# Kernel optimization log

Hardware: AMD Instinct MI355X
Metric: run time of the kernel (lower is better)

## Reference

```python
import jax, jax.numpy as jnp
import numpy as np

WIN = 7
NUM_HEADS = 12
DIM = 384
HEAD_DIM = DIM // NUM_HEADS
SEQ = WIN * WIN


def _relative_position_index():
    ch, cw = np.meshgrid(np.arange(WIN), np.arange(WIN), indexing='ij')
    coords = np.stack([ch, cw]).reshape(2, -1)            # [2, 49]
    rel = coords[:, :, None] - coords[:, None, :]          # [2, 49, 49]
    rel = rel.transpose(1, 2, 0)
    rel[:, :, 0] += WIN - 1
    rel[:, :, 1] += WIN - 1
    rel[:, :, 0] *= 2 * WIN - 1
    return rel.sum(-1).astype(np.int32)                    # [49, 49]


def setup_inputs() -> dict:
    key = jax.random.key(0)
    ks = jax.random.split(key, 12)
    bz = 2048
    mw = 64  # windows per image
    s = 0.02
    inp = {
        'hidden_states': jax.random.normal(ks[0], (bz, SEQ, DIM), jnp.float32),
        'attention_mask': jax.random.normal(ks[1], (mw, SEQ, SEQ), jnp.float32),
        'qW': jax.random.normal(ks[2], (DIM, DIM), jnp.float32) * s,
        'qb': jnp.zeros((DIM,), jnp.float32),
        'kW': jax.random.normal(ks[3], (DIM, DIM), jnp.float32) * s,
        'kb': jnp.zeros((DIM,), jnp.float32),
        'vW': jax.random.normal(ks[4], (DIM, DIM), jnp.float32) * s,
        'vb': jnp.zeros((DIM,), jnp.float32),
        'oW': jax.random.normal(ks[5], (DIM, DIM), jnp.float32) * s,
        'ob': jnp.zeros((DIM,), jnp.float32),
        'bias_table': jax.random.normal(ks[6], ((2 * WIN - 1) ** 2, NUM_HEADS), jnp.float32) * s,
        'rel_idx': jnp.asarray(_relative_position_index()),
    }
    return inp


def reference(hidden_states, attention_mask, qW, qb, kW, kb, vW, vb, oW, ob, bias_table, rel_idx):
    bz, seq, dim = hidden_states.shape
    H, D = NUM_HEADS, HEAD_DIM

    def heads(x, W, b):
        y = jnp.einsum('bsd,de->bse', hidden_states, W) + b
        return y.reshape(bz, seq, H, D).transpose(0, 2, 1, 3)  # [b, h, s, d]

    q = heads(hidden_states, qW, qb)
    k = heads(hidden_states, kW, kb)
    v = heads(hidden_states, vW, vb)

    scores = jnp.einsum('bhsd,bhtd->bhst', q, k) / jnp.sqrt(jnp.float32(D))

    # relative position bias: gather [49*49, H] -> [H, 49, 49]
    rpb = bias_table[rel_idx.reshape(-1)].reshape(seq, seq, H).transpose(2, 0, 1)
    scores = scores + rpb[None]

    mw = attention_mask.shape[0]
    scores = scores.reshape(bz // mw, mw, H, seq, seq) + attention_mask[None, :, None]
    scores = scores.reshape(bz, H, seq, seq)

    attn = jax.nn.softmax(scores, axis=-1)
    ctx = jnp.einsum('bhst,bhtd->bhsd', attn, v)
    ctx = ctx.transpose(0, 2, 1, 3).reshape(bz, seq, dim)
    return jnp.einsum('bsd,de->bse', ctx, oW) + ob
```

## Files before the change

### kernel.cpp

```cpp
#include <hip/hip_runtime.h>


typedef unsigned short u16;
typedef unsigned int   u32;
typedef short bf16x8 __attribute__((ext_vector_type(8)));
typedef float f32x4  __attribute__((ext_vector_type(4)));
typedef u16   u16x8  __attribute__((ext_vector_type(8)));
typedef u16   u16x4  __attribute__((ext_vector_type(4)));

#define NWIN   2048
#define SEQ    49
#define DIM    384
#define NH     12
#define HD     32
#define MTOT   (NWIN*SEQ)
#define WELEM  (DIM*DIM)

__device__ __forceinline__ u16 f2b(float f) {
    union { float f; unsigned u; } c; c.f = f;
    unsigned u = c.u;
    u += 0x7FFFu + ((u >> 16) & 1u);
    return (u16)(u >> 16);
}

__global__ __launch_bounds__(256) void prep_x(const float* __restrict__ X, u16* __restrict__ Xb) {
    int i = blockIdx.x * 256 + threadIdx.x;
    float4 v = ((const float4*)X)[i];
    u16x4 o; o[0]=f2b(v.x); o[1]=f2b(v.y); o[2]=f2b(v.z); o[3]=f2b(v.w);
    ((u16x4*)Xb)[i] = o;
}

__global__ __launch_bounds__(256) void prep_w(const float* __restrict__ qW, const float* __restrict__ kW,
                                              const float* __restrict__ vW, const float* __restrict__ oW,
                                              u16* __restrict__ Wt) {
    int t = blockIdx.x * 256 + threadIdx.x;
    int m = t / WELEM; int rem = t - m * WELEM;
    int k = rem / DIM; int n = rem - k * DIM;
    const float* src = (m==0) ? qW : (m==1) ? kW : (m==2) ? vW : oW;
    Wt[m*WELEM + n*DIM + k] = f2b(src[rem]);
}

__global__ __launch_bounds__(256) void prep_rpb(const float* __restrict__ bt, const int* __restrict__ ridx,
                                                float* __restrict__ rpb) {
    int t = blockIdx.x * 256 + threadIdx.x;
    if (t >= NH * SEQ * SEQ) return;
    int h = t / (SEQ*SEQ); int st = t - h * (SEQ*SEQ);
    rpb[t] = bt[ridx[st] * NH + h];
}

__device__ __forceinline__ void gload_lds16(const void* g, void* l) {
    __builtin_amdgcn_global_load_lds((const __attribute__((address_space(1))) void*)g,
                                     (__attribute__((address_space(3))) void*)l, 16, 0, 0);
}

__device__ __forceinline__ void stage_tile_async(const u16* __restrict__ g0, u16* lds, int wv, int lane) {
    const int r8   = lane >> 3;
    const int scol = ((lane & 7) * 8) ^ (r8 << 3);
    const u16* src = g0 + (wv * 8 + r8) * DIM + scol;
    u16*       dst = lds + wv * 512 + lane * 8;
    #pragma unroll
    for (int i = 0; i < 4; i++)
        gload_lds16(src + i * 32 * DIM, dst + i * 2048);
}

__device__ __forceinline__ void gemm_tile(const u16* __restrict__ Abase, const u16* __restrict__ Bbase,
                                          f32x4 (&acc)[4][4]) {
    __shared__ __align__(16) u16 As[128 * 64];
    __shared__ __align__(16) u16 Bs[128 * 64];
    const int tid = threadIdx.x, wave = tid >> 6, lane = tid & 63;
    const int wm = wave >> 1, wn = wave & 1;
    const int swzl = (lane & 7) << 3;
    for (int kt = 0; kt < 6; kt++) {
        __syncthreads();
        stage_tile_async(Abase + kt * 64, As, wave, lane);
        stage_tile_async(Bbase + kt * 64, Bs, wave, lane);
        __syncthreads();
        #pragma unroll
        for (int kk = 0; kk < 2; kk++) {
            const int co = (kk * 32 + (lane >> 4) * 8) ^ swzl;
            bf16x8 a[4], b[4];
            #pragma unroll
            for (int mi = 0; mi < 4; mi++)
                a[mi] = *(const bf16x8*)&As[(wm * 64 + mi * 16 + (lane & 15)) * 64 + co];
            #pragma unroll
            for (int ni = 0; ni < 4; ni++)
                b[ni] = *(const bf16x8*)&Bs[(wn * 64 + ni * 16 + (lane & 15)) * 64 + co];
            #pragma unroll
            for (int mi = 0; mi < 4; mi++)
                #pragma unroll
                for (int ni = 0; ni < 4; ni++)
                    acc[mi][ni] = __builtin_amdgcn_mfma_f32_16x16x32_bf16(a[mi], b[ni], acc[mi][ni], 0, 0, 0);
        }
    }
}

__global__ __launch_bounds__(256) void qkv_gemm(const u16* __restrict__ Xb, const u16* __restrict__ Wt,
                                                const float* __restrict__ qb, const float* __restrict__ kb,
                                                const float* __restrict__ vb,
                                                u16* __restrict__ Qo, u16* __restrict__ Ko, u16* __restrict__ Vo) {
    const int bid = blockIdx.x;
    const int swz = (bid & 7) * 882 + (bid >> 3);
    const int mTile = swz / 9, p = swz - mTile * 9;
    const int mBase = mTile * 128;
    const int proj = p / 3, nBase = (p - proj * 3) * 128;
    f32x4 acc[4][4];
    #pragma unroll
    for (int mi = 0; mi < 4; mi++)
        #pragma unroll
        for (int ni = 0; ni < 4; ni++) { f32x4 z = {0.f,0.f,0.f,0.f}; acc[mi][ni] = z; }

    gemm_tile(Xb + mBase * DIM, Wt + proj * WELEM + nBase * DIM, acc);

    const float* bias = (proj==0) ? qb : (proj==1) ? kb : vb;
    u16* Out          = (proj==0) ? Qo : (proj==1) ? Ko : Vo;
    const float scale = (proj==0) ? 0.17677669529663687f : 1.0f;
    const int tid = threadIdx.x, wave = tid >> 6, lane = tid & 63;
    const int wm = wave >> 1, wn = wave & 1;

    float bias4[4]; int hh[4], dd[4];
    #pragma unroll
    for (int ni = 0; ni < 4; ni++) {
        int nin = nBase + wn * 64 + ni * 16 + (lane & 15);
        bias4[ni] = bias[nin]; hh[ni] = nin >> 5; dd[ni] = nin & 31;
    }
    #pragma unroll
    for (int mi = 0; mi < 4; mi++) {
        #pragma unroll
        for (int j = 0; j < 4; j++) {
            int gm = mBase + wm * 64 + mi * 16 + ((lane >> 4) << 2) + j;
            int bw = gm / SEQ, s = gm - bw * SEQ;
            int rowbase = (bw * (NH*SEQ) + s) * HD;
            #pragma unroll
            for (int ni = 0; ni < 4; ni++) {
                float val = (acc[mi][ni][j] + bias4[ni]) * scale;
                Out[rowbase + hh[ni] * (SEQ*HD) + dd[ni]] = f2b(val);
            }
        }
    }
}

__global__ __launch_bounds__(256) void attn_mfma(const u16* __restrict__ Qb, const u16* __restrict__ Kb,
                                                 const u16* __restrict__ Vb, const float* __restrict__ rpb,
                                                 const float* __restrict__ mask, u16* __restrict__ Ctx) {
    const int wm = blockIdx.x;
    const int h  = blockIdx.y;
    const int jg = blockIdx.z;
    const int tid = threadIdx.x, wv = tid >> 6, lane = tid & 63;
    const int r16 = lane & 15, g = lane >> 4;

    __shared__ float comb[64][68];
    {
        const float* rp = rpb + h * (SEQ*SEQ);
        const float* mp = mask + wm * (SEQ*SEQ);
        for (int idx = tid; idx < 64*64; idx += 256) {
            int s = idx >> 6, t = idx & 63;
            float v = -1e30f;
            if (s < SEQ && t < SEQ) v = rp[s*SEQ + t] + mp[s*SEQ + t];
            comb[s][t] = v;
        }
    }
    __syncthreads();

    const int j = jg * 4 + wv;
    const int w = j * 64 + wm;
    const u16* Qp = Qb + (w*NH + h) * (SEQ*HD);
    const u16* Kp = Kb + (w*NH + h) * (SEQ*HD);
    const u16* Vp = Vb + (w*NH + h) * (SEQ*HD);

    bf16x8 kf[4], qf[4];
    #pragma unroll
    for (int ti = 0; ti < 4; ti++) kf[ti] = *(const bf16x8*)&Kp[(ti*16 + r16)*HD + g*8];
    #pragma unroll
    for (int si = 0; si < 4; si++) qf[si] = *(const bf16x8*)&Qp[(si*16 + r16)*HD + g*8];

    f32x4 st[4][4];
    #pragma unroll
    for (int ti = 0; ti < 4; ti++)
        #pragma unroll
        for (int si = 0; si < 4; si++) {
            f32x4 z = {0.f,0.f,0.f,0.f};
            st[ti][si] = __builtin_amdgcn_mfma_f32_16x16x32_bf16(kf[ti], qf[si], z, 0, 0, 0);
        }

    #pragma unroll
    for (int ti = 0; ti < 4; ti++)
        #pragma unroll
        for (int si = 0; si < 4; si++) {
            const float4 c = *(const float4*)&comb[si*16 + r16][ti*16 + g*4];
            st[ti][si][0] += c.x; st[ti][si][1] += c.y; st[ti][si][2] += c.z; st[ti][si][3] += c.w;
        }

    #pragma unroll
    for (int si = 0; si < 4; si++) {
        float m = st[0][si][0];
        #pragma unroll
        for (int ti = 0; ti < 4; ti++)
            #pragma unroll
            for (int r = 0; r < 4; r++) m = fmaxf(m, st[ti][si][r]);
        m = fmaxf(m, __shfl_xor(m, 16));
        m = fmaxf(m, __shfl_xor(m, 32));
        float sum = 0.f;
        #pragma unroll
        for (int ti = 0; ti < 4; ti++)
            #pragma unroll
            for (int r = 0; r < 4; r++) {
                float p = __expf(st[ti][si][r] - m);
                st[ti][si][r] = p; sum += p;
            }
        sum += __shfl_xor(sum, 16);
        sum += __shfl_xor(sum, 32);
        float rs = 1.0f / sum;
        #pragma unroll
        for (int ti = 0; ti < 4; ti++)
            #pragma unroll
            for (int r = 0; r < 4; r++) st[ti][si][r] *= rs;
    }

    u32 pk[4][4][2];
    #pragma unroll
    for (int ti = 0; ti < 4; ti++)
        #pragma unroll
        for (int si = 0; si < 4; si++)
            #pragma unroll
            for (int q = 0; q < 2; q++) {
                u32 r;
                asm("v_cvt_pk_bf16_f32 %0, %1, %2" : "=v"(r) : "v"(st[ti][si][2*q]), "v"(st[ti][si][2*q+1]));
                pk[ti][si][q] = r;
            }

    bf16x8 pa[2][4];
    const int base_src = r16 + ((g & 1) << 5);
    #pragma unroll
    for (int kc = 0; kc < 2; kc++)
        #pragma unroll
        for (int si = 0; si < 4; si++) {
            union { u32 u[4]; bf16x8 v; } cv;
            #pragma unroll
            for (int jj = 0; jj < 4; jj++) {
                int srcl = base_src + ((jj >> 1) << 4);
                u32 x0 = (u32)__shfl((int)pk[kc*2 + 0][si][jj & 1], srcl);
                u32 x1 = (u32)__shfl((int)pk[kc*2 + 1][si][jj & 1], srcl);
                cv.u[jj] = (lane >= 32) ? x1 : x0;
            }
            pa[kc][si] = cv.v;
        }

    bf16x8 vf[2][2];
    #pragma unroll
    for (int kc = 0; kc < 2; kc++)
        #pragma unroll
        for (int nt = 0; nt < 2; nt++) {
            bf16x8 v;
            #pragma unroll
            for (int i = 0; i < 8; i++)
                v[i] = (short)Vp[(kc*32 + g*8 + i)*HD + nt*16 + r16];
            vf[kc][nt] = v;
        }

    f32x4 ct[4][2];
    #pragma unroll
    for (int si = 0; si < 4; si++)
        #pragma unroll
        for (int nt = 0; nt < 2; nt++) {
            f32x4 z = {0.f,0.f,0.f,0.f};
            z = __builtin_amdgcn_mfma_f32_16x16x32_bf16(pa[0][si], vf[0][nt], z, 0, 0, 0);
            ct[si][nt] = __builtin_amdgcn_mfma_f32_16x16x32_bf16(pa[1][si], vf[1][nt], z, 0, 0, 0);
        }

    #pragma unroll
    for (int si = 0; si < 4; si++)
        #pragma unroll
        for (int r = 0; r < 4; r++) {
            int s = si*16 + g*4 + r;
            if (s < SEQ) {
                #pragma unroll
                for (int nt = 0; nt < 2; nt++)
                    Ctx[(w*SEQ + s)*DIM + h*HD + nt*16 + r16] = f2b(ct[si][nt][r]);
            }
        }
}

__global__ __launch_bounds__(256) void oproj_gemm(const u16* __restrict__ Cb, const u16* __restrict__ Wo,
                                                  const float* __restrict__ ob, float* __restrict__ out) {
    const int bid = blockIdx.x;
    const int swz = (bid & 7) * 294 + (bid >> 3);
    const int mTile = swz / 3, nTile = swz - mTile * 3;
    const int mBase = mTile * 128, nBase = nTile * 128;
    f32x4 acc[4][4];
    #pragma unroll
    for (int mi = 0; mi < 4; mi++)
        #pragma unroll
        for (int ni = 0; ni < 4; ni++) { f32x4 z = {0.f,0.f,0.f,0.f}; acc[mi][ni] = z; }

    gemm_tile(Cb + mBase * DIM, Wo + nBase * DIM, acc);

    const int tid = threadIdx.x, wave = tid >> 6, lane = tid & 63;
    const int wm = wave >> 1, wn = wave & 1;
    float ob4[4]; int gn4[4];
    #pragma unroll
    for (int ni = 0; ni < 4; ni++) {
        gn4[ni] = nBase + wn * 64 + ni * 16 + (lane & 15);
        ob4[ni] = ob[gn4[ni]];
    }
    #pragma unroll
    for (int mi = 0; mi < 4; mi++) {
        #pragma unroll
        for (int j = 0; j < 4; j++) {
            int gm = mBase + wm * 64 + mi * 16 + ((lane >> 4) << 2) + j;
            #pragma unroll
            for (int ni = 0; ni < 4; ni++)
                out[gm * DIM + gn4[ni]] = acc[mi][ni][j] + ob4[ni];
        }
    }
}

extern "C" void kernel_launch(void* const* d_in, const int* in_sizes, int n_in,
                              void* d_out, int out_size, void* d_ws, size_t ws_size,
                              hipStream_t stream) {
    const float* hs   = (const float*)d_in[0];
    const float* mask = (const float*)d_in[1];
    const float* qW   = (const float*)d_in[2];
    const float* qb   = (const float*)d_in[3];
    const float* kW   = (const float*)d_in[4];
    const float* kb   = (const float*)d_in[5];
    const float* vW   = (const float*)d_in[6];
    const float* vb   = (const float*)d_in[7];
    const float* oW   = (const float*)d_in[8];
    const float* ob   = (const float*)d_in[9];
    const float* bt   = (const float*)d_in[10];
    const int*   ridx = (const int*)d_in[11];
    float* out = (float*)d_out;

    char* ws = (char*)d_ws;
    u16* Xb   = (u16*)(ws);
    u16* Ctx  = (u16*)(ws);
    u16* Qb   = (u16*)(ws + 77070336);
    u16* Kb   = (u16*)(ws + 154140672);
    u16* Vb   = (u16*)(ws + 231211008);
    u16* Wt   = (u16*)(ws + 308281344);
    float* rpb = (float*)(ws + 309460992);

    prep_x  <<<37632, 256, 0, stream>>>(hs, Xb);
    prep_w  <<<2304, 256, 0, stream>>>(qW, kW, vW, oW, Wt);
    prep_rpb<<<113, 256, 0, stream>>>(bt, ridx, rpb);
    qkv_gemm<<<7056, 256, 0, stream>>>(Xb, Wt, qb, kb, vb, Qb, Kb, Vb);
    attn_mfma<<<dim3(64, NH, 8), 256, 0, stream>>>(Qb, Kb, Vb, rpb, mask, Ctx);
    oproj_gemm<<<2352, 256, 0, stream>>>(Ctx, Wt + 3 * WELEM, ob, out);
}
```

Baseline: 353.3 us.

## Fuse fp32-to-bf16 input conversion into QKV GEMM and enlarge GEMM tiles to 256 rows

```diff
diff --git a/kernel.cpp b/kernel.cpp
--- a/kernel.cpp
+++ b/kernel.cpp
@@ -21,13 +21,6 @@
     unsigned u = c.u;
     u += 0x7FFFu + ((u >> 16) & 1u);
     return (u16)(u >> 16);
-}
-
-__global__ __launch_bounds__(256) void prep_x(const float* __restrict__ X, u16* __restrict__ Xb) {
-    int i = blockIdx.x * 256 + threadIdx.x;
-    float4 v = ((const float4*)X)[i];
-    u16x4 o; o[0]=f2b(v.x); o[1]=f2b(v.y); o[2]=f2b(v.z); o[3]=f2b(v.w);
-    ((u16x4*)Xb)[i] = o;
 }
 
 __global__ __launch_bounds__(256) void prep_w(const float* __restrict__ qW, const float* __restrict__ kW,
@@ -53,55 +46,103 @@
                                      (__attribute__((address_space(3))) void*)l, 16, 0, 0);
 }
 
-__device__ __forceinline__ void stage_tile_async(const u16* __restrict__ g0, u16* lds, int wv, int lane) {
-    const int r8   = lane >> 3;
-    const int scol = ((lane & 7) * 8) ^ (r8 << 3);
-    const u16* src = g0 + (wv * 8 + r8) * DIM + scol;
-    u16*       dst = lds + wv * 512 + lane * 8;
-    #pragma unroll
-    for (int i = 0; i < 4; i++)
-        gload_lds16(src + i * 32 * DIM, dst + i * 2048);
-}
-
-__device__ __forceinline__ void gemm_tile(const u16* __restrict__ Abase, const u16* __restrict__ Bbase,
-                                          f32x4 (&acc)[4][4]) {
-    __shared__ __align__(16) u16 As[128 * 64];
+__device__ __forceinline__ void mfma_step(const u16* As, const u16* Bs, int wm, int wn, int lane,
+                                          int swzl, f32x4 (&acc)[4][4]) {
+    #pragma unroll
+    for (int kk = 0; kk < 2; kk++) {
+        const int co = (kk * 32 + (lane >> 4) * 8) ^ swzl;
+        bf16x8 a[4], b[4];
+        #pragma unroll
+        for (int mi = 0; mi < 4; mi++)
+            a[mi] = *(const bf16x8*)&As[(wm * 64 + mi * 16 + (lane & 15)) * 64 + co];
+        #pragma unroll
+        for (int ni = 0; ni < 4; ni++)
+            b[ni] = *(const bf16x8*)&Bs[(wn * 64 + ni * 16 + (lane & 15)) * 64 + co];
+        #pragma unroll
+        for (int mi = 0; mi < 4; mi++)
+            #pragma unroll
+            for (int ni = 0; ni < 4; ni++)
+                acc[mi][ni] = __builtin_amdgcn_mfma_f32_16x16x32_bf16(a[mi], b[ni], acc[mi][ni], 0, 0, 0);
+    }
+}
+
+__device__ __forceinline__ void gemm_tile_qkv(const float* __restrict__ Af, const u16* __restrict__ Bbase,
+                                              f32x4 (&acc)[4][4]) {
+    __shared__ __align__(16) u16 As[256 * 64];
     __shared__ __align__(16) u16 Bs[128 * 64];
     const int tid = threadIdx.x, wave = tid >> 6, lane = tid & 63;
     const int wm = wave >> 1, wn = wave & 1;
     const int swzl = (lane & 7) << 3;
+    const int r8 = lane >> 3;
+    const int scol = ((lane & 7) * 8) ^ (r8 << 3);
+    const int arow = tid >> 1, ahalf = (tid & 1) * 32;
+    const int aswz = (arow & 7) << 3;
+    const float* arow_p = Af + arow * DIM;
+
     for (int kt = 0; kt < 6; kt++) {
         __syncthreads();
-        stage_tile_async(Abase + kt * 64, As, wave, lane);
-        stage_tile_async(Bbase + kt * 64, Bs, wave, lane);
+        #pragma unroll
+        for (int i = 0; i < 2; i++) {
+            int c = i * 8 + wave;
+            gload_lds16(Bbase + kt * 64 + (c * 8 + r8) * DIM + scol, Bs + c * 512 + lane * 8);
+        }
+        const float* asrc = arow_p + kt * 64 + ahalf;
+        #pragma unroll
+        for (int hq = 0; hq < 2; hq++) {
+            union { u32 u[4]; u16x8 v; } lo, hi;
+            #pragma unroll
+            for (int q = 0; q < 2; q++) {
+                float4 v0 = *(const float4*)(asrc + hq * 16 + q * 4);
+                float4 v1 = *(const float4*)(asrc + hq * 16 + 8 + q * 4);
+                asm("v_cvt_pk_bf16_f32 %0, %1, %2" : "=v"(lo.u[2*q+0]) : "v"(v0.x), "v"(v0.y));
+                asm("v_cvt_pk_bf16_f32 %0, %1, %2" : "=v"(lo.u[2*q+1]) : "v"(v0.z), "v"(v0.w));
+                asm("v_cvt_pk_bf16_f32 %0, %1, %2" : "=v"(hi.u[2*q+0]) : "v"(v1.x), "v"(v1.y));
+                asm("v_cvt_pk_bf16_f32 %0, %1, %2" : "=v"(hi.u[2*q+1]) : "v"(v1.z), "v"(v1.w));
+            }
+            const int c0 = ahalf + hq * 16;
+            *(u16x8*)&As[arow * 64 + ((c0    ) ^ aswz)] = lo.v;
+            *(u16x8*)&As[arow * 64 + ((c0 + 8) ^ aswz)] = hi.v;
+        }
         __syncthreads();
-        #pragma unroll
-        for (int kk = 0; kk < 2; kk++) {
-            const int co = (kk * 32 + (lane >> 4) * 8) ^ swzl;
-            bf16x8 a[4], b[4];
-            #pragma unroll
-            for (int mi = 0; mi < 4; mi++)
-                a[mi] = *(const bf16x8*)&As[(wm * 64 + mi * 16 + (lane & 15)) * 64 + co];
-            #pragma unroll
-            for (int ni = 0; ni < 4; ni++)
-                b[ni] = *(const bf16x8*)&Bs[(wn * 64 + ni * 16 + (lane & 15)) * 64 + co];
-            #pragma unroll
-            for (int mi = 0; mi < 4; mi++)
-                #pragma unroll
-                for (int ni = 0; ni < 4; ni++)
-                    acc[mi][ni] = __builtin_amdgcn_mfma_f32_16x16x32_bf16(a[mi], b[ni], acc[mi][ni], 0, 0, 0);
-        }
-    }
-}
-
-__global__ __launch_bounds__(256) void qkv_gemm(const u16* __restrict__ Xb, const u16* __restrict__ Wt,
-                                                const float* __restrict__ qb, const float* __restrict__ kb,
-                                                const float* __restrict__ vb,
-                                                u16* __restrict__ Qo, u16* __restrict__ Ko, u16* __restrict__ Vo) {
+        mfma_step(As, Bs, wm, wn, lane, swzl, acc);
+    }
+}
+
+__device__ __forceinline__ void gemm_tile_o(const u16* __restrict__ Abase, const u16* __restrict__ Bbase,
+                                            f32x4 (&acc)[4][4]) {
+    __shared__ __align__(16) u16 As[256 * 64];
+    __shared__ __align__(16) u16 Bs[128 * 64];
+    const int tid = threadIdx.x, wave = tid >> 6, lane = tid & 63;
+    const int wm = wave >> 1, wn = wave & 1;
+    const int swzl = (lane & 7) << 3;
+    const int r8 = lane >> 3;
+    const int scol = ((lane & 7) * 8) ^ (r8 << 3);
+
+    for (int kt = 0; kt < 6; kt++) {
+        __syncthreads();
+        #pragma unroll
+        for (int i = 0; i < 4; i++) {
+            int c = i * 8 + wave;
+            gload_lds16(Abase + kt * 64 + (c * 8 + r8) * DIM + scol, As + c * 512 + lane * 8);
+        }
+        #pragma unroll
+        for (int i = 0; i < 2; i++) {
+            int c = i * 8 + wave;
+            gload_lds16(Bbase + kt * 64 + (c * 8 + r8) * DIM + scol, Bs + c * 512 + lane * 8);
+        }
+        __syncthreads();
+        mfma_step(As, Bs, wm, wn, lane, swzl, acc);
+    }
+}
+
+__global__ __launch_bounds__(512, 4) void qkv_gemm(const float* __restrict__ X, const u16* __restrict__ Wt,
+                                                   const float* __restrict__ qb, const float* __restrict__ kb,
+                                                   const float* __restrict__ vb,
+                                                   u16* __restrict__ Qo, u16* __restrict__ Ko, u16* __restrict__ Vo) {
     const int bid = blockIdx.x;
-    const int swz = (bid & 7) * 882 + (bid >> 3);
+    const int swz = (bid & 7) * 441 + (bid >> 3);
     const int mTile = swz / 9, p = swz - mTile * 9;
-    const int mBase = mTile * 128;
+    const int mBase = mTile * 256;
     const int proj = p / 3, nBase = (p - proj * 3) * 128;
     f32x4 acc[4][4];
     #pragma unroll
@@ -109,7 +150,7 @@
         #pragma unroll
         for (int ni = 0; ni < 4; ni++) { f32x4 z = {0.f,0.f,0.f,0.f}; acc[mi][ni] = z; }
 
-    gemm_tile(Xb + mBase * DIM, Wt + proj * WELEM + nBase * DIM, acc);
+    gemm_tile_qkv(X + mBase * DIM, Wt + proj * WELEM + nBase * DIM, acc);
 
     const float* bias = (proj==0) ? qb : (proj==1) ? kb : vb;
     u16* Out          = (proj==0) ? Qo : (proj==1) ? Ko : Vo;
@@ -280,19 +321,19 @@
         }
 }
 
-__global__ __launch_bounds__(256) void oproj_gemm(const u16* __restrict__ Cb, const u16* __restrict__ Wo,
-                                                  const float* __restrict__ ob, float* __restrict__ out) {
+__global__ __launch_bounds__(512, 4) void oproj_gemm(const u16* __restrict__ Cb, const u16* __restrict__ Wo,
+                                                     const float* __restrict__ ob, float* __restrict__ out) {
     const int bid = blockIdx.x;
-    const int swz = (bid & 7) * 294 + (bid >> 3);
+    const int swz = (bid & 7) * 147 + (bid >> 3);
     const int mTile = swz / 3, nTile = swz - mTile * 3;
-    const int mBase = mTile * 128, nBase = nTile * 128;
+    const int mBase = mTile * 256, nBase = nTile * 128;
     f32x4 acc[4][4];
     #pragma unroll
     for (int mi = 0; mi < 4; mi++)
         #pragma unroll
         for (int ni = 0; ni < 4; ni++) { f32x4 z = {0.f,0.f,0.f,0.f}; acc[mi][ni] = z; }
 
-    gemm_tile(Cb + mBase * DIM, Wo + nBase * DIM, acc);
+    gemm_tile_o(Cb + mBase * DIM, Wo + nBase * DIM, acc);
 
     const int tid = threadIdx.x, wave = tid >> 6, lane = tid & 63;
     const int wm = wave >> 1, wn = wave & 1;
@@ -332,7 +373,6 @@
     float* out = (float*)d_out;
 
     char* ws = (char*)d_ws;
-    u16* Xb   = (u16*)(ws);
     u16* Ctx  = (u16*)(ws);
     u16* Qb   = (u16*)(ws + 77070336);
     u16* Kb   = (u16*)(ws + 154140672);
@@ -340,10 +380,9 @@
     u16* Wt   = (u16*)(ws + 308281344);
     float* rpb = (float*)(ws + 309460992);
 
-    prep_x  <<<37632, 256, 0, stream>>>(hs, Xb);
     prep_w  <<<2304, 256, 0, stream>>>(qW, kW, vW, oW, Wt);
     prep_rpb<<<113, 256, 0, stream>>>(bt, ridx, rpb);
-    qkv_gemm<<<7056, 256, 0, stream>>>(Xb, Wt, qb, kb, vb, Qb, Kb, Vb);
+    qkv_gemm<<<3528, 512, 0, stream>>>(hs, Wt, qb, kb, vb, Qb, Kb, Vb);
     attn_mfma<<<dim3(64, NH, 8), 256, 0, stream>>>(Qb, Kb, Vb, rpb, mask, Ctx);
-    oproj_gemm<<<2352, 256, 0, stream>>>(Ctx, Wt + 3 * WELEM, ob, out);
-}
+    oproj_gemm<<<1176, 512, 0, stream>>>(Ctx, Wt + 3 * WELEM, ob, out);
+}
```

After: 442.4 us. 25.2% more time.

## Precompute combined bias+mask table and stage V through LDS per wave

Applied to the files above, without the earlier changes.

```diff
diff --git a/kernel.cpp b/kernel.cpp
--- a/kernel.cpp
+++ b/kernel.cpp
@@ -40,12 +40,18 @@
     Wt[m*WELEM + n*DIM + k] = f2b(src[rem]);
 }
 
-__global__ __launch_bounds__(256) void prep_rpb(const float* __restrict__ bt, const int* __restrict__ ridx,
-                                                float* __restrict__ rpb) {
-    int t = blockIdx.x * 256 + threadIdx.x;
-    if (t >= NH * SEQ * SEQ) return;
-    int h = t / (SEQ*SEQ); int st = t - h * (SEQ*SEQ);
-    rpb[t] = bt[ridx[st] * NH + h];
+__global__ __launch_bounds__(256) void prep_comb(const float* __restrict__ bt, const int* __restrict__ ridx,
+                                                 const float* __restrict__ mask, float* __restrict__ comb) {
+    int idx = blockIdx.x * 256 + threadIdx.x;
+    int t = idx & 63, s = (idx >> 6) & 63;
+    int hw = idx >> 12;
+    int h = hw % NH, wm = hw / NH;
+    float v = -1e30f;
+    if (s < SEQ && t < SEQ) {
+        int st = s * SEQ + t;
+        v = bt[ridx[st] * NH + h] + mask[wm * (SEQ*SEQ) + st];
+    }
+    comb[idx] = v;
 }
 
 __device__ __forceinline__ void gload_lds16(const void* g, void* l) {
@@ -140,32 +146,30 @@
 }
 
 __global__ __launch_bounds__(256) void attn_mfma(const u16* __restrict__ Qb, const u16* __restrict__ Kb,
-                                                 const u16* __restrict__ Vb, const float* __restrict__ rpb,
-                                                 const float* __restrict__ mask, u16* __restrict__ Ctx) {
-    const int wm = blockIdx.x;
-    const int h  = blockIdx.y;
-    const int jg = blockIdx.z;
+                                                 const u16* __restrict__ Vb, const float* __restrict__ comb,
+                                                 u16* __restrict__ Ctx) {
     const int tid = threadIdx.x, wv = tid >> 6, lane = tid & 63;
     const int r16 = lane & 15, g = lane >> 4;
-
-    __shared__ float comb[64][68];
+    const int idx = blockIdx.x * 4 + wv;
+    const int w = idx / NH, h = idx - w * NH;
+    const int wm = w & 63;
+
+    __shared__ __align__(16) u16 vlds[4][64 * HD];
+
+    const u16* Qp = Qb + idx * (SEQ*HD);
+    const u16* Kp = Kb + idx * (SEQ*HD);
+    const u16* Vp = Vb + idx * (SEQ*HD);
+
     {
-        const float* rp = rpb + h * (SEQ*SEQ);
-        const float* mp = mask + wm * (SEQ*SEQ);
-        for (int idx = tid; idx < 64*64; idx += 256) {
-            int s = idx >> 6, t = idx & 63;
-            float v = -1e30f;
-            if (s < SEQ && t < SEQ) v = rp[s*SEQ + t] + mp[s*SEQ + t];
-            comb[s][t] = v;
-        }
-    }
-    __syncthreads();
-
-    const int j = jg * 4 + wv;
-    const int w = j * 64 + wm;
-    const u16* Qp = Qb + (w*NH + h) * (SEQ*HD);
-    const u16* Kp = Kb + (w*NH + h) * (SEQ*HD);
-    const u16* Vp = Vb + (w*NH + h) * (SEQ*HD);
+        u16x8 z8 = {0,0,0,0,0,0,0,0};
+        #pragma unroll
+        for (int c4 = 0; c4 < 4; c4++) {
+            int c = c4 * 64 + lane;
+            u16x8 val = z8;
+            if ((c >> 2) < SEQ) val = *(const u16x8*)&Vp[c * 8];
+            *(u16x8*)&vlds[wv][c * 8] = val;
+        }
+    }
 
     bf16x8 kf[4], qf[4];
     #pragma unroll
@@ -174,6 +178,7 @@
     for (int si = 0; si < 4; si++) qf[si] = *(const bf16x8*)&Qp[(si*16 + r16)*HD + g*8];
 
     f32x4 st[4][4];
+    __builtin_amdgcn_s_setprio(1);
     #pragma unroll
     for (int ti = 0; ti < 4; ti++)
         #pragma unroll
@@ -181,12 +186,14 @@
             f32x4 z = {0.f,0.f,0.f,0.f};
             st[ti][si] = __builtin_amdgcn_mfma_f32_16x16x32_bf16(kf[ti], qf[si], z, 0, 0, 0);
         }
-
+    __builtin_amdgcn_s_setprio(0);
+
+    const float* cp = comb + (size_t)(wm * NH + h) * 4096;
     #pragma unroll
     for (int ti = 0; ti < 4; ti++)
         #pragma unroll
         for (int si = 0; si < 4; si++) {
-            const float4 c = *(const float4*)&comb[si*16 + r16][ti*16 + g*4];
+            const float4 c = *(const float4*)&cp[(si*16 + r16) * 64 + ti*16 + g*4];
             st[ti][si][0] += c.x; st[ti][si][1] += c.y; st[ti][si][2] += c.z; st[ti][si][3] += c.w;
         }
 
@@ -253,11 +260,12 @@
             bf16x8 v;
             #pragma unroll
             for (int i = 0; i < 8; i++)
-                v[i] = (short)Vp[(kc*32 + g*8 + i)*HD + nt*16 + r16];
+                v[i] = (short)vlds[wv][(kc*32 + g*8 + i)*HD + nt*16 + r16];
             vf[kc][nt] = v;
         }
 
     f32x4 ct[4][2];
+    __builtin_amdgcn_s_setprio(1);
     #pragma unroll
     for (int si = 0; si < 4; si++)
         #pragma unroll
@@ -266,6 +274,7 @@
             z = __builtin_amdgcn_mfma_f32_16x16x32_bf16(pa[0][si], vf[0][nt], z, 0, 0, 0);
             ct[si][nt] = __builtin_amdgcn_mfma_f32_16x16x32_bf16(pa[1][si], vf[1][nt], z, 0, 0, 0);
         }
+    __builtin_amdgcn_s_setprio(0);
 
     #pragma unroll
     for (int si = 0; si < 4; si++)
@@ -338,12 +347,12 @@
     u16* Kb   = (u16*)(ws + 154140672);
     u16* Vb   = (u16*)(ws + 231211008);
     u16* Wt   = (u16*)(ws + 308281344);
-    float* rpb = (float*)(ws + 309460992);
-
-    prep_x  <<<37632, 256, 0, stream>>>(hs, Xb);
-    prep_w  <<<2304, 256, 0, stream>>>(qW, kW, vW, oW, Wt);
-    prep_rpb<<<113, 256, 0, stream>>>(bt, ridx, rpb);
-    qkv_gemm<<<7056, 256, 0, stream>>>(Xb, Wt, qb, kb, vb, Qb, Kb, Vb);
-    attn_mfma<<<dim3(64, NH, 8), 256, 0, stream>>>(Qb, Kb, Vb, rpb, mask, Ctx);
+    float* comb = (float*)(ws + 309460992);
+
+    prep_x   <<<37632, 256, 0, stream>>>(hs, Xb);
+    prep_w   <<<2304, 256, 0, stream>>>(qW, kW, vW, oW, Wt);
+    prep_comb<<<12288, 256, 0, stream>>>(bt, ridx, mask, comb);
+    qkv_gemm <<<7056, 256, 0, stream>>>(Xb, Wt, qb, kb, vb, Qb, Kb, Vb);
+    attn_mfma<<<6144, 256, 0, stream>>>(Qb, Kb, Vb, comb, Ctx);
     oproj_gemm<<<2352, 256, 0, stream>>>(Ctx, Wt + 3 * WELEM, ob, out);
 }
```

Measured after the change: 378.1 us. 1.07x slower.
